# Kernel optimization log

Measured on AMD Instinct MI355X. Metric: run time of the kernel, lower is better.

## Reference

```python
import jax, jax.numpy as jnp
import numpy as np

HIDDEN = 1024
HEADS = 16
HEAD_DIM = HIDDEN // HEADS  # 64
MLP_HIDDEN = int(HIDDEN * 4.0)  # 4096
B, L = 2, 2048
EPS_LN = 1e-6
EPS_RMS = 1e-6


def setup_inputs() -> dict:
    key = jax.random.key(0)
    ks = jax.random.split(key, 12)
    s = 0.02
    return {
        "x": jax.random.normal(ks[0], (B, L, HIDDEN), jnp.float32),
        "vec": jax.random.normal(ks[1], (B, HIDDEN), jnp.float32),
        "pe": jax.random.normal(ks[2], (1, 1, L, HEAD_DIM // 2, 2, 2), jnp.float32),
        "w_mod": jax.random.normal(ks[3], (HIDDEN, 3 * HIDDEN), jnp.float32) * s,
        "b_mod": jnp.zeros((3 * HIDDEN,), jnp.float32),
        "w1": jax.random.normal(ks[4], (HIDDEN, 3 * HIDDEN + MLP_HIDDEN), jnp.float32) * s,
        "b1": jnp.zeros((3 * HIDDEN + MLP_HIDDEN,), jnp.float32),
        "w_mlp": jax.random.normal(ks[5], (MLP_HIDDEN, HIDDEN), jnp.float32) * s,
        "b_mlp": jnp.zeros((HIDDEN,), jnp.float32),
        "w2": jax.random.normal(ks[6], (2 * HIDDEN, HIDDEN), jnp.float32) * s,
        "b2": jnp.zeros((HIDDEN,), jnp.float32),
        "q_scale": jnp.ones((HEAD_DIM,), jnp.float32),
        "k_scale": jnp.ones((HEAD_DIM,), jnp.float32),
    }


def _layernorm(x, eps=EPS_LN):
    m = jnp.mean(x, axis=-1, keepdims=True)
    v = jnp.mean(jnp.square(x - m), axis=-1, keepdims=True)
    return (x - m) * jax.lax.rsqrt(v + eps)


def _rmsnorm(x, scale, eps=EPS_RMS):
    rrms = jax.lax.rsqrt(jnp.mean(jnp.square(x), axis=-1, keepdims=True) + eps)
    return x * rrms * scale


def _apply_rope(t, pe):
    # t: [B,H,L,D]; pe: [1,1,L,D//2,2,2]
    t_ = t.reshape(*t.shape[:-1], -1, 1, 2)  # [B,H,L,D//2,1,2]
    out = pe[..., 0] * t_[..., 0] + pe[..., 1] * t_[..., 1]  # [B,H,L,D//2,2]
    return out.reshape(t.shape)


def reference(x, vec, pe, w_mod, b_mod, w1, b1, w_mlp, b_mlp, w2, b2, q_scale, k_scale):
    # adaLN modulation: silu(vec) -> Dense(3*dim) -> shift, scale, gate
    mod = (jax.nn.silu(vec) @ w_mod + b_mod)[:, None, :]  # [B,1,3H]
    shift, scale, gate = jnp.split(mod, 3, axis=-1)
    x_mod = (1.0 + scale) * _layernorm(x) + shift
    # fused QKV + MLP projection
    h = x_mod @ w1 + b1  # [B,L,3H+MH]
    qkv, mlp = h[..., : 3 * HIDDEN], h[..., 3 * HIDDEN :]
    qkv = qkv.reshape(x.shape[0], x.shape[1], 3, HEADS, HEAD_DIM)
    qkv = jnp.transpose(qkv, (2, 0, 3, 1, 4))  # [3,B,H,L,D]
    q, k, v = qkv[0], qkv[1], qkv[2]
    # QK-RMSNorm per head-dim
    q = _rmsnorm(q, q_scale)
    k = _rmsnorm(k, k_scale)
    # RoPE
    q = _apply_rope(q, pe)
    k = _apply_rope(k, pe)
    # attention
    scores = jnp.einsum("bhqd,bhkd->bhqk", q, k) * (HEAD_DIM ** -0.5)
    probs = jax.nn.softmax(scores, axis=-1)
    attn = jnp.einsum("bhqk,bhkd->bhqd", probs, v)
    attn = jnp.transpose(attn, (0, 2, 1, 3)).reshape(x.shape[0], x.shape[1], HIDDEN)
    # mlp branch (Dense with tanh activation per source) + fused output proj
    mlp_out = jnp.tanh(mlp @ w_mlp + b_mlp)
    out = jnp.concatenate([attn, mlp_out], axis=-1) @ w2 + b2
    return x + gate * out
```

## Files before the change

### kernel.cpp

```cpp
#include <hip/hip_runtime.h>
#include <stdint.h>


#define HID  1024
#define NH   16
#define HD   64
#define MLP  4096
#define D1   7168
#define DQKV 3072
#define DCAT 2048
#define BB   2
#define LL   2048
#define TOK  4096

typedef __attribute__((ext_vector_type(8))) short    bf16x8;
typedef __attribute__((ext_vector_type(4))) float    f32x4;
typedef __attribute__((ext_vector_type(4))) unsigned int u32x4;

__device__ __forceinline__ float b2f(unsigned short u) {
    unsigned int v = ((unsigned int)u) << 16;
    float f; __builtin_memcpy(&f, &v, 4); return f;
}
__device__ __forceinline__ unsigned short f2b(float f) {
    unsigned int v; __builtin_memcpy(&v, &f, 4);
    unsigned int r = (v + 0x7FFFu + ((v >> 16) & 1u)) >> 16;
    return (unsigned short)r;
}
__device__ __forceinline__ unsigned int pkbf2(float a, float b) {
    unsigned int ua, ub;
    __builtin_memcpy(&ua, &a, 4); __builtin_memcpy(&ub, &b, 4);
    return ((ua + 0x8000u) >> 16) | ((ub + 0x8000u) & 0xFFFF0000u);
}
__device__ __forceinline__ void gl_lds16(const unsigned short* g, unsigned short* l) {
    __builtin_amdgcn_global_load_lds(
        (const __attribute__((address_space(1))) unsigned int*)(g),
        (__attribute__((address_space(3))) unsigned int*)(l), 16, 0, 0);
}

__global__ void k_transpose_cvt(const float* __restrict__ in,
                                unsigned short* __restrict__ out, int R, int C) {
    __shared__ float tile[32][33];
    int bx = blockIdx.x, by = blockIdx.y;
    int tx = threadIdx.x, ty = threadIdx.y;
    #pragma unroll
    for (int i = 0; i < 4; i++) {
        int r = by * 32 + ty + i * 8;
        int c = bx * 32 + tx;
        tile[ty + i * 8][tx] = in[(size_t)r * C + c];
    }
    __syncthreads();
    #pragma unroll
    for (int i = 0; i < 4; i++) {
        int ro = bx * 32 + ty + i * 8;
        int co = by * 32 + tx;
        out[(size_t)ro * R + co] = f2b(tile[tx][ty + i * 8]);
    }
}

__global__ void k_vt(const unsigned short* __restrict__ h,
                     unsigned short* __restrict__ vT) {
    __shared__ unsigned short tile[32][33];
    int l0 = blockIdx.x * 32;
    int d0 = (blockIdx.y & 1) * 32;
    int bh = blockIdx.y >> 1;
    int b = bh >> 4, hh = bh & 15;
    int tx = threadIdx.x, ty = threadIdx.y;
    const unsigned short* src = h + ((size_t)(b * LL) + l0) * D1 + 2 * HID + hh * HD + d0;
    #pragma unroll
    for (int i = 0; i < 4; i++)
        tile[ty + i * 8][tx] = src[(size_t)(ty + i * 8) * D1 + tx];
    __syncthreads();
    unsigned short* dst = vT + ((size_t)(b * NH + hh) * HD + d0) * LL + l0;
    #pragma unroll
    for (int i = 0; i < 4; i++)
        dst[(size_t)(ty + i * 8) * LL + tx] = tile[tx][ty + i * 8];
}

__global__ void k_mod(const float* __restrict__ vec,
                      const float* __restrict__ w_mod,
                      const float* __restrict__ b_mod,
                      float* __restrict__ mod) {
    __shared__ float sv[HID];
    __shared__ float red[8][32];
    int b = blockIdx.y, t = threadIdx.x;
    for (int j = t; j < HID; j += 256) {
        float v = vec[b * HID + j];
        sv[j] = v / (1.0f + __expf(-v));
    }
    __syncthreads();
    int n0 = blockIdx.x * 32;
    int on = t & 31, ks = t >> 5;
    float acc = 0.f;
    const float* wp = w_mod + (size_t)(ks * 128) * 3072 + n0 + on;
    #pragma unroll 4
    for (int k = 0; k < 128; k++) acc += sv[ks * 128 + k] * wp[(size_t)k * 3072];
    red[ks][on] = acc;
    __syncthreads();
    if (t < 32) {
        float s = 0.f;
        #pragma unroll
        for (int i = 0; i < 8; i++) s += red[i][t];
        mod[b * 3072 + n0 + t] = s + b_mod[n0 + t];
    }
}

__global__ void k_lnmod(const float* __restrict__ x,
                        const float* __restrict__ mod,
                        unsigned short* __restrict__ xmod) {
    int tok = blockIdx.x;
    int t = threadIdx.x;
    int b = tok >> 11;
    float4 v4 = *(const float4*)(x + (size_t)tok * HID + t * 4);
    float v0 = v4.x, v1 = v4.y, v2 = v4.z, v3 = v4.w;
    float s  = v0 + v1 + v2 + v3;
    float sq = v0*v0 + v1*v1 + v2*v2 + v3*v3;
    for (int off = 1; off < 64; off <<= 1) {
        s  += __shfl_xor(s,  off);
        sq += __shfl_xor(sq, off);
    }
    __shared__ float ls[4], lq[4];
    int w = t >> 6;
    if ((t & 63) == 0) { ls[w] = s; lq[w] = sq; }
    __syncthreads();
    s  = ls[0] + ls[1] + ls[2] + ls[3];
    sq = lq[0] + lq[1] + lq[2] + lq[3];
    float mean = s * (1.0f / HID);
    float var  = sq * (1.0f / HID) - mean * mean;
    float rstd = rsqrtf(var + 1e-6f);
    const float* mb = mod + b * 3072;
    float y[4] = {v0, v1, v2, v3};
    unsigned short r[4];
    #pragma unroll
    for (int j = 0; j < 4; j++) {
        int col = t * 4 + j;
        float nval = (y[j] - mean) * rstd;
        r[j] = f2b((1.0f + mb[1024 + col]) * nval + mb[col]);
    }
    unsigned int o0 = (unsigned int)r[0] | ((unsigned int)r[1] << 16);
    unsigned int o1 = (unsigned int)r[2] | ((unsigned int)r[3] << 16);
    *(uint2*)(xmod + (size_t)tok * HID + t * 4) = make_uint2(o0, o1);
}

template<int EPI>
__global__ __launch_bounds__(256) void k_gemm(
    const unsigned short* __restrict__ A, int lda,
    const unsigned short* __restrict__ Bt, int ldb,
    const float* __restrict__ bias,
    unsigned short* __restrict__ C, float* __restrict__ Cf, int ldc,
    int K,
    const float* __restrict__ xin,
    const float* __restrict__ mod) {
    __shared__ alignas(16) unsigned short As[128 * 64];
    __shared__ alignas(16) unsigned short Bs[128 * 64];
    int t = threadIdx.x;
    int bm = blockIdx.x, bn = blockIdx.y;
    int lane = t & 63, wave = t >> 6;
    int wm = (wave >> 1) * 64, wn = (wave & 1) * 64;
    int ln = lane & 15, quad = lane >> 4;
    int ln7 = ln & 7;

    f32x4 acc[4][4];
    #pragma unroll
    for (int i = 0; i < 4; i++)
        #pragma unroll
        for (int j = 0; j < 4; j++) acc[i][j] = {0.f, 0.f, 0.f, 0.f};

    int sr  = t >> 3;
    int scg = (t & 7) ^ (sr & 7);
    const unsigned short* Ab = A  + (size_t)(bm * 128) * lda;
    const unsigned short* Bb = Bt + (size_t)(bn * 128) * ldb;

    int ksplit = K / gridDim.z;
    int kbeg = blockIdx.z * ksplit, kend = kbeg + ksplit;

    for (int k0 = kbeg; k0 < kend; k0 += 64) {
        __syncthreads();
        #pragma unroll
        for (int c = 0; c < 4; c++) {
            gl_lds16(Ab + (size_t)(c * 32 + sr) * lda + k0 + scg * 8, &As[c * 2048 + t * 8]);
            gl_lds16(Bb + (size_t)(c * 32 + sr) * ldb + k0 + scg * 8, &Bs[c * 2048 + t * 8]);
        }
        __syncthreads();
        #pragma unroll
        for (int ks = 0; ks < 2; ks++) {
            int slot = ((ks * 4 + quad) ^ ln7) * 8;
            bf16x8 af[4], bfr[4];
            #pragma unroll
            for (int i = 0; i < 4; i++)
                af[i] = *(const bf16x8*)(&As[(wm + i * 16 + ln) * 64 + slot]);
            #pragma unroll
            for (int j = 0; j < 4; j++)
                bfr[j] = *(const bf16x8*)(&Bs[(wn + j * 16 + ln) * 64 + slot]);
            #pragma unroll
            for (int i = 0; i < 4; i++)
                #pragma unroll
                for (int j = 0; j < 4; j++)
                    acc[i][j] = __builtin_amdgcn_mfma_f32_16x16x32_bf16(bfr[j], af[i], acc[i][j], 0, 0, 0);
        }
    }

    #pragma unroll
    for (int i = 0; i < 4; i++) {
        #pragma unroll
        for (int j = 0; j < 4; j++) {
            int trow = bm * 128 + wm + i * 16 + ln;
            int ncol = bn * 128 + wn + j * 16 + quad * 4;
            f32x4 a = acc[i][j];
            if (EPI == 3) {
                float4 o = make_float4(a[0], a[1], a[2], a[3]);
                *(float4*)(&Cf[((size_t)blockIdx.z * TOK + trow) * ldc + ncol]) = o;
            } else {
                float4 bv = *(const float4*)(bias + ncol);
                float v0 = a[0] + bv.x, v1 = a[1] + bv.y, v2 = a[2] + bv.z, v3 = a[3] + bv.w;
                if (EPI == 1) { v0 = tanhf(v0); v1 = tanhf(v1); v2 = tanhf(v2); v3 = tanhf(v3); }
                if (EPI == 0 || EPI == 1) {
                    *(uint2*)(&C[(size_t)trow * ldc + ncol]) =
                        make_uint2(pkbf2(v0, v1), pkbf2(v2, v3));
                } else {
                    int b = trow >> 11;
                    float4 gv = *(const float4*)(mod + b * 3072 + 2048 + ncol);
                    float4 xv = *(const float4*)(xin + (size_t)trow * HID + ncol);
                    float4 o = make_float4(xv.x + gv.x * v0, xv.y + gv.y * v1,
                                           xv.z + gv.z * v2, xv.w + gv.w * v3);
                    *(float4*)(&Cf[(size_t)trow * ldc + ncol]) = o;
                }
            }
        }
    }
}

__global__ __launch_bounds__(256) void k_red1(const float* __restrict__ part,
                                              const float* __restrict__ bias,
                                              unsigned short* __restrict__ cat) {
    int idx = blockIdx.x * 256 + threadIdx.x;
    int row = idx >> 8;
    int c4  = (idx & 255) * 4;
    float4 p0 = *(const float4*)(part + (size_t)row * HID + c4);
    float4 p1 = *(const float4*)(part + ((size_t)TOK + row) * HID + c4);
    float4 bv = *(const float4*)(bias + c4);
    float a0 = tanhf(p0.x + p1.x + bv.x);
    float a1 = tanhf(p0.y + p1.y + bv.y);
    float a2 = tanhf(p0.z + p1.z + bv.z);
    float a3 = tanhf(p0.w + p1.w + bv.w);
    *(uint2*)(&cat[(size_t)row * DCAT + HID + c4]) =
        make_uint2(pkbf2(a0, a1), pkbf2(a2, a3));
}

__global__ __launch_bounds__(256) void k_red2(const float* __restrict__ part,
                                              const float* __restrict__ bias,
                                              const float* __restrict__ x,
                                              const float* __restrict__ mod,
                                              float* __restrict__ out) {
    int idx = blockIdx.x * 256 + threadIdx.x;
    int row = idx >> 8;
    int c4  = (idx & 255) * 4;
    int b = row >> 11;
    float4 p0 = *(const float4*)(part + (size_t)row * HID + c4);
    float4 p1 = *(const float4*)(part + ((size_t)TOK + row) * HID + c4);
    float4 bv = *(const float4*)(bias + c4);
    float4 gv = *(const float4*)(mod + b * 3072 + 2048 + c4);
    float4 xv = *(const float4*)(x + (size_t)row * HID + c4);
    float4 o;
    o.x = xv.x + gv.x * (p0.x + p1.x + bv.x);
    o.y = xv.y + gv.y * (p0.y + p1.y + bv.y);
    o.z = xv.z + gv.z * (p0.z + p1.z + bv.z);
    o.w = xv.w + gv.w * (p0.w + p1.w + bv.w);
    *(float4*)(out + (size_t)row * HID + c4) = o;
}

__global__ void k_qkrope(unsigned short* __restrict__ h,
                         const float* __restrict__ pe,
                         const float* __restrict__ q_scale,
                         const float* __restrict__ k_scale) {
    int tok = blockIdx.x;
    int l = tok & (LL - 1);
    int t = threadIdx.x;
    int lane = t & 63, wave = t >> 6;
    int hh = wave * 4 + (lane >> 4);
    int d0 = (lane & 15) * 4;
    unsigned short* row = h + (size_t)tok * D1;
    int i0 = d0 >> 1;
    const float* peb = pe + ((size_t)l * 32 + i0) * 4;
    float4 e0 = *(const float4*)(peb);
    float4 e1 = *(const float4*)(peb + 4);
    #pragma unroll
    for (int qk = 0; qk < 2; qk++) {
        unsigned short* p = row + qk * HID + hh * HD + d0;
        const float* sc = (qk == 0 ? q_scale : k_scale) + d0;
        uint2 qv = *(const uint2*)p;
        float v0 = b2f((unsigned short)(qv.x & 0xFFFF)), v1 = b2f((unsigned short)(qv.x >> 16));
        float v2 = b2f((unsigned short)(qv.y & 0xFFFF)), v3 = b2f((unsigned short)(qv.y >> 16));
        float ssq = v0*v0 + v1*v1 + v2*v2 + v3*v3;
        ssq += __shfl_xor(ssq, 1, 16);
        ssq += __shfl_xor(ssq, 2, 16);
        ssq += __shfl_xor(ssq, 4, 16);
        ssq += __shfl_xor(ssq, 8, 16);
        float rr = rsqrtf(ssq * (1.0f / HD) + 1e-6f);
        if (qk == 0) rr *= 0.18033688011112042f;
        v0 *= rr * sc[0];
        v1 *= rr * sc[1];
        v2 *= rr * sc[2];
        v3 *= rr * sc[3];
        float o0 = e0.x*v0 + e0.y*v1;
        float o1 = e0.z*v0 + e0.w*v1;
        float o2 = e1.x*v2 + e1.y*v3;
        float o3 = e1.z*v2 + e1.w*v3;
        *(uint2*)p = make_uint2(pkbf2(o0, o1), pkbf2(o2, o3));
    }
}

#define KT 64
#define LDP 72
__global__ __launch_bounds__(256) void k_attn(const unsigned short* __restrict__ h,
                                              const unsigned short* __restrict__ vT,
                                              unsigned short* __restrict__ cat) {
    __shared__ alignas(16) unsigned short Ks[KT * 64];
    __shared__ alignas(16) unsigned short Vs[HD * 64];
    __shared__ unsigned short Ps[4 * 16 * LDP];
    int t = threadIdx.x;
    int bx = blockIdx.x;
    int bh = blockIdx.y;
    int b = bh >> 4, hh = bh & 15;
    int lane = t & 63, w = t >> 6;
    int ln = lane & 15, quad = lane >> 4;
    int ln7 = ln & 7;
    const unsigned short* hb = h + (size_t)b * LL * D1;
    const unsigned short* vtb = vT + ((size_t)(b * NH + hh) * HD) * LL;

    bf16x8 qf[2];
    {
        const unsigned short* qbase = hb + (size_t)(bx * 64 + w * 16) * D1 + hh * HD;
        #pragma unroll
        for (int ks = 0; ks < 2; ks++)
            qf[ks] = *(const bf16x8*)(qbase + (size_t)ln * D1 + ks * 32 + quad * 8);
    }

    f32x4 O[4];
    #pragma unroll
    for (int vn = 0; vn < 4; vn++) O[vn] = {0.f, 0.f, 0.f, 0.f};
    float m_ = -1e30f, l_ = 0.f;

    unsigned short* Psw = Ps + w * 16 * LDP;

    int srow = t >> 3;
    int scg  = (t & 7) ^ (srow & 7);

    for (int kb = 0; kb < LL / KT; kb++) {
        __syncthreads();
        {
            const unsigned short* kb0 = hb + (size_t)(kb * KT) * D1 + HID + hh * HD;
            gl_lds16(kb0 + (size_t)srow * D1 + scg * 8,        &Ks[t * 8]);
            gl_lds16(kb0 + (size_t)(srow + 32) * D1 + scg * 8, &Ks[2048 + t * 8]);
            const unsigned short* vb0 = vtb + kb * KT;
            gl_lds16(vb0 + (size_t)srow * LL + scg * 8,        &Vs[t * 8]);
            gl_lds16(vb0 + (size_t)(srow + 32) * LL + scg * 8, &Vs[2048 + t * 8]);
        }
        __syncthreads();

        f32x4 st[4];
        #pragma unroll
        for (int kt = 0; kt < 4; kt++) {
            st[kt] = {0.f, 0.f, 0.f, 0.f};
            #pragma unroll
            for (int ks = 0; ks < 2; ks++) {
                bf16x8 kf = *(const bf16x8*)(&Ks[(kt * 16 + ln) * 64 + (((ks * 4 + quad) ^ ln7) * 8)]);
                st[kt] = __builtin_amdgcn_mfma_f32_16x16x32_bf16(kf, qf[ks], st[kt], 0, 0, 0);
            }
        }

        {
            float p[16];
            float mx = -1e30f;
            #pragma unroll
            for (int kt = 0; kt < 4; kt++)
                #pragma unroll
                for (int r = 0; r < 4; r++) {
                    float v = st[kt][r];
                    p[kt * 4 + r] = v;
                    mx = fmaxf(mx, v);
                }
            mx = fmaxf(mx, __shfl_xor(mx, 16));
            mx = fmaxf(mx, __shfl_xor(mx, 32));
            float mnew = fmaxf(m_, mx);
            float alpha = __builtin_amdgcn_exp2f(m_ - mnew);
            m_ = mnew;
            float sum = 0.f;
            #pragma unroll
            for (int i = 0; i < 16; i++) {
                float e = __builtin_amdgcn_exp2f(p[i] - mnew);
                p[i] = e;
                sum += e;
            }
            sum += __shfl_xor(sum, 16);
            sum += __shfl_xor(sum, 32);
            l_ = l_ * alpha + sum;
            #pragma unroll
            for (int vn = 0; vn < 4; vn++)
                #pragma unroll
                for (int r = 0; r < 4; r++) O[vn][r] *= alpha;
            #pragma unroll
            for (int kt = 0; kt < 4; kt++) {
                unsigned long long pk =
                    (unsigned long long)pkbf2(p[kt*4+0], p[kt*4+1])
                  | ((unsigned long long)pkbf2(p[kt*4+2], p[kt*4+3]) << 32);
                *(unsigned long long*)(&Psw[ln * LDP + kt * 16 + quad * 4]) = pk;
            }
        }

        #pragma unroll
        for (int kt2 = 0; kt2 < 2; kt2++) {
            bf16x8 pb = *(const bf16x8*)(&Psw[ln * LDP + kt2 * 32 + quad * 8]);
            #pragma unroll
            for (int vn = 0; vn < 4; vn++) {
                bf16x8 vf = *(const bf16x8*)(&Vs[(vn * 16 + ln) * 64 + (((kt2 * 4 + quad) ^ ln7) * 8)]);
                O[vn] = __builtin_amdgcn_mfma_f32_16x16x32_bf16(vf, pb, O[vn], 0, 0, 0);
            }
        }
    }

    {
        float rl = 1.0f / l_;
        size_t row = (size_t)(b * LL + bx * 64 + w * 16 + ln);
        #pragma unroll
        for (int vn = 0; vn < 4; vn++) {
            #pragma unroll
            for (int r2 = 0; r2 < 4; r2 += 2) {
                unsigned int pk = pkbf2(O[vn][r2] * rl, O[vn][r2 + 1] * rl);
                *(unsigned int*)(&cat[row * DCAT + hh * HD + vn * 16 + quad * 4 + r2]) = pk;
            }
        }
    }
}

extern "C" void kernel_launch(void* const* d_in, const int* in_sizes, int n_in,
                              void* d_out, int out_size, void* d_ws, size_t ws_size,
                              hipStream_t stream) {
    const float* x       = (const float*)d_in[0];
    const float* vec     = (const float*)d_in[1];
    const float* pe      = (const float*)d_in[2];
    const float* w_mod   = (const float*)d_in[3];
    const float* b_mod   = (const float*)d_in[4];
    const float* w1      = (const float*)d_in[5];
    const float* b1      = (const float*)d_in[6];
    const float* w_mlp   = (const float*)d_in[7];
    const float* b_mlp   = (const float*)d_in[8];
    const float* w2      = (const float*)d_in[9];
    const float* b2      = (const float*)d_in[10];
    const float* q_scale = (const float*)d_in[11];
    const float* k_scale = (const float*)d_in[12];
    float* out = (float*)d_out;

    char* ws = (char*)d_ws;
    size_t off = 0;
    float* mod = (float*)(ws + off);                     off += 6144 * 4;
    unsigned short* xmod  = (unsigned short*)(ws + off); off += (size_t)TOK * HID * 2;
    unsigned short* h     = (unsigned short*)(ws + off); off += (size_t)TOK * D1 * 2;
    unsigned short* cat   = (unsigned short*)(ws + off); off += (size_t)TOK * DCAT * 2;
    unsigned short* w1T   = (unsigned short*)(ws + off); off += (size_t)D1 * HID * 2;
    unsigned short* wmlpT = (unsigned short*)(ws + off); off += (size_t)HID * MLP * 2;
    unsigned short* w2T   = (unsigned short*)(ws + off); off += (size_t)HID * DCAT * 2;
    unsigned short* vTr   = (unsigned short*)(ws + off); off += (size_t)BB * NH * HD * LL * 2;
    float* part = (float*)(ws + off);                    off += (size_t)2 * TOK * HID * 4;

    k_transpose_cvt<<<dim3(D1 / 32, HID / 32), dim3(32, 8), 0, stream>>>(w1, w1T, HID, D1);
    k_transpose_cvt<<<dim3(HID / 32, MLP / 32), dim3(32, 8), 0, stream>>>(w_mlp, wmlpT, MLP, HID);
    k_transpose_cvt<<<dim3(HID / 32, DCAT / 32), dim3(32, 8), 0, stream>>>(w2, w2T, DCAT, HID);

    k_mod<<<dim3(96, BB), 256, 0, stream>>>(vec, w_mod, b_mod, mod);
    k_lnmod<<<TOK, 256, 0, stream>>>(x, mod, xmod);

    k_gemm<0><<<dim3(TOK / 128, D1 / 128), 256, 0, stream>>>(
        xmod, HID, w1T, HID, b1, h, nullptr, D1, HID, nullptr, nullptr);

    k_vt<<<dim3(LL / 32, 2 * BB * NH), dim3(32, 8), 0, stream>>>(h, vTr);
    k_qkrope<<<TOK, 256, 0, stream>>>(h, pe, q_scale, k_scale);

    k_attn<<<dim3(LL / 64, BB * NH), 256, 0, stream>>>(h, vTr, cat);

    k_gemm<3><<<dim3(TOK / 128, HID / 128, 2), 256, 0, stream>>>(
        h + DQKV, D1, wmlpT, MLP, b_mlp, nullptr, part, HID, MLP, nullptr, nullptr);
    k_red1<<<TOK * HID / 1024, 256, 0, stream>>>(part, b_mlp, cat);

    k_gemm<3><<<dim3(TOK / 128, HID / 128, 2), 256, 0, stream>>>(
        cat, DCAT, w2T, DCAT, b2, nullptr, part, HID, DCAT, nullptr, nullptr);
    k_red2<<<TOK * HID / 1024, 256, 0, stream>>>(part, b2, x, mod, out);
}
```

Baseline: 429.0 us.

## Fuse QK RMSNorm, RoPE and V transpose into QKV GEMM epilogue

The first projection GEMM gains a dedicated epilogue that adds bias, then applies per-head RMSNorm and RoPE to the Q and K column blocks in registers. It writes V directly in transposed layout and stores the MLP part normally. This removes the separate V-transpose and qk-rope kernels along with their extra passes over the large h buffer. In exchange, the transposed V stores are strided 2-byte writes, and the epilogue adds register pressure and branching.

```diff
diff --git a/kernel.cpp b/kernel.cpp
--- a/kernel.cpp
+++ b/kernel.cpp
@@ -55,25 +55,6 @@
         int co = by * 32 + tx;
         out[(size_t)ro * R + co] = f2b(tile[tx][ty + i * 8]);
     }
-}
-
-__global__ void k_vt(const unsigned short* __restrict__ h,
-                     unsigned short* __restrict__ vT) {
-    __shared__ unsigned short tile[32][33];
-    int l0 = blockIdx.x * 32;
-    int d0 = (blockIdx.y & 1) * 32;
-    int bh = blockIdx.y >> 1;
-    int b = bh >> 4, hh = bh & 15;
-    int tx = threadIdx.x, ty = threadIdx.y;
-    const unsigned short* src = h + ((size_t)(b * LL) + l0) * D1 + 2 * HID + hh * HD + d0;
-    #pragma unroll
-    for (int i = 0; i < 4; i++)
-        tile[ty + i * 8][tx] = src[(size_t)(ty + i * 8) * D1 + tx];
-    __syncthreads();
-    unsigned short* dst = vT + ((size_t)(b * NH + hh) * HD + d0) * LL + l0;
-    #pragma unroll
-    for (int i = 0; i < 4; i++)
-        dst[(size_t)(ty + i * 8) * LL + tx] = tile[tx][ty + i * 8];
 }
 
 __global__ void k_mod(const float* __restrict__ vec,
@@ -149,7 +130,11 @@
     unsigned short* __restrict__ C, float* __restrict__ Cf, int ldc,
     int K,
     const float* __restrict__ xin,
-    const float* __restrict__ mod) {
+    const float* __restrict__ mod,
+    unsigned short* __restrict__ vT,
+    const float* __restrict__ pe,
+    const float* __restrict__ q_scale,
+    const float* __restrict__ k_scale) {
     __shared__ alignas(16) unsigned short As[128 * 64];
     __shared__ alignas(16) unsigned short Bs[128 * 64];
     int t = threadIdx.x;
@@ -197,6 +182,86 @@
                 for (int j = 0; j < 4; j++)
                     acc[i][j] = __builtin_amdgcn_mfma_f32_16x16x32_bf16(bfr[j], af[i], acc[i][j], 0, 0, 0);
         }
+    }
+
+    if (EPI == 4) {
+        #pragma unroll
+        for (int j = 0; j < 4; j++) {
+            int ncol = bn * 128 + wn + j * 16 + quad * 4;
+            float4 bv = *(const float4*)(bias + ncol);
+            #pragma unroll
+            for (int i = 0; i < 4; i++) {
+                acc[i][j][0] += bv.x; acc[i][j][1] += bv.y;
+                acc[i][j][2] += bv.z; acc[i][j][3] += bv.w;
+            }
+        }
+        int region = bn >> 3;
+        if (region <= 1) {
+            const float* scp = (region == 0) ? q_scale : k_scale;
+            float4 sc4[4];
+            #pragma unroll
+            for (int j = 0; j < 4; j++)
+                sc4[j] = *(const float4*)(scp + j * 16 + quad * 4);
+            #pragma unroll
+            for (int i = 0; i < 4; i++) {
+                int trow = bm * 128 + wm + i * 16 + ln;
+                int l = trow & (LL - 1);
+                float ssq = 0.f;
+                #pragma unroll
+                for (int j = 0; j < 4; j++)
+                    #pragma unroll
+                    for (int r = 0; r < 4; r++) ssq += acc[i][j][r] * acc[i][j][r];
+                ssq += __shfl_xor(ssq, 16);
+                ssq += __shfl_xor(ssq, 32);
+                float rr = rsqrtf(ssq * (1.0f / HD) + 1e-6f);
+                if (region == 0) rr *= 0.18033688011112042f;
+                #pragma unroll
+                for (int j = 0; j < 4; j++) {
+                    float v0 = acc[i][j][0] * rr * sc4[j].x;
+                    float v1 = acc[i][j][1] * rr * sc4[j].y;
+                    float v2 = acc[i][j][2] * rr * sc4[j].z;
+                    float v3 = acc[i][j][3] * rr * sc4[j].w;
+                    const float* peb = pe + ((size_t)l * 32 + j * 8 + quad * 2) * 4;
+                    float4 e0 = *(const float4*)(peb);
+                    float4 e1 = *(const float4*)(peb + 4);
+                    float o0 = e0.x * v0 + e0.y * v1;
+                    float o1 = e0.z * v0 + e0.w * v1;
+                    float o2 = e1.x * v2 + e1.y * v3;
+                    float o3 = e1.z * v2 + e1.w * v3;
+                    int ncol = bn * 128 + wn + j * 16 + quad * 4;
+                    *(uint2*)(&C[(size_t)trow * ldc + ncol]) =
+                        make_uint2(pkbf2(o0, o1), pkbf2(o2, o3));
+                }
+            }
+        } else if (region == 2) {
+            int hh = (bn * 128 + wn - 2048) >> 6;
+            #pragma unroll
+            for (int i = 0; i < 4; i++) {
+                int trow = bm * 128 + wm + i * 16 + ln;
+                int b = trow >> 11, l = trow & (LL - 1);
+                unsigned short* dstb = vT + ((size_t)(b * NH + hh) * HD) * LL + l;
+                #pragma unroll
+                for (int j = 0; j < 4; j++) {
+                    int d0 = j * 16 + quad * 4;
+                    #pragma unroll
+                    for (int r = 0; r < 4; r++)
+                        dstb[(size_t)(d0 + r) * LL] = f2b(acc[i][j][r]);
+                }
+            }
+        } else {
+            #pragma unroll
+            for (int i = 0; i < 4; i++) {
+                int trow = bm * 128 + wm + i * 16 + ln;
+                #pragma unroll
+                for (int j = 0; j < 4; j++) {
+                    int ncol = bn * 128 + wn + j * 16 + quad * 4;
+                    *(uint2*)(&C[(size_t)trow * ldc + ncol]) =
+                        make_uint2(pkbf2(acc[i][j][0], acc[i][j][1]),
+                                   pkbf2(acc[i][j][2], acc[i][j][3]));
+                }
+            }
+        }
+        return;
     }
 
     #pragma unroll
@@ -213,7 +278,7 @@
                 float4 bv = *(const float4*)(bias + ncol);
                 float v0 = a[0] + bv.x, v1 = a[1] + bv.y, v2 = a[2] + bv.z, v3 = a[3] + bv.w;
                 if (EPI == 1) { v0 = tanhf(v0); v1 = tanhf(v1); v2 = tanhf(v2); v3 = tanhf(v3); }
-                if (EPI == 0 || EPI == 1) {
+                if (EPI == 1) {
                     *(uint2*)(&C[(size_t)trow * ldc + ncol]) =
                         make_uint2(pkbf2(v0, v1), pkbf2(v2, v3));
                 } else {
@@ -268,47 +333,6 @@
     *(float4*)(out + (size_t)row * HID + c4) = o;
 }
 
-__global__ void k_qkrope(unsigned short* __restrict__ h,
-                         const float* __restrict__ pe,
-                         const float* __restrict__ q_scale,
-                         const float* __restrict__ k_scale) {
-    int tok = blockIdx.x;
-    int l = tok & (LL - 1);
-    int t = threadIdx.x;
-    int lane = t & 63, wave = t >> 6;
-    int hh = wave * 4 + (lane >> 4);
-    int d0 = (lane & 15) * 4;
-    unsigned short* row = h + (size_t)tok * D1;
-    int i0 = d0 >> 1;
-    const float* peb = pe + ((size_t)l * 32 + i0) * 4;
-    float4 e0 = *(const float4*)(peb);
-    float4 e1 = *(const float4*)(peb + 4);
-    #pragma unroll
-    for (int qk = 0; qk < 2; qk++) {
-        unsigned short* p = row + qk * HID + hh * HD + d0;
-        const float* sc = (qk == 0 ? q_scale : k_scale) + d0;
-        uint2 qv = *(const uint2*)p;
-        float v0 = b2f((unsigned short)(qv.x & 0xFFFF)), v1 = b2f((unsigned short)(qv.x >> 16));
-        float v2 = b2f((unsigned short)(qv.y & 0xFFFF)), v3 = b2f((unsigned short)(qv.y >> 16));
-        float ssq = v0*v0 + v1*v1 + v2*v2 + v3*v3;
-        ssq += __shfl_xor(ssq, 1, 16);
-        ssq += __shfl_xor(ssq, 2, 16);
-        ssq += __shfl_xor(ssq, 4, 16);
-        ssq += __shfl_xor(ssq, 8, 16);
-        float rr = rsqrtf(ssq * (1.0f / HD) + 1e-6f);
-        if (qk == 0) rr *= 0.18033688011112042f;
-        v0 *= rr * sc[0];
-        v1 *= rr * sc[1];
-        v2 *= rr * sc[2];
-        v3 *= rr * sc[3];
-        float o0 = e0.x*v0 + e0.y*v1;
-        float o1 = e0.z*v0 + e0.w*v1;
-        float o2 = e1.x*v2 + e1.y*v3;
-        float o3 = e1.z*v2 + e1.w*v3;
-        *(uint2*)p = make_uint2(pkbf2(o0, o1), pkbf2(o2, o3));
-    }
-}
-
 #define KT 64
 #define LDP 72
 __global__ __launch_bounds__(256) void k_attn(const unsigned short* __restrict__ h,
@@ -469,19 +493,19 @@
     k_mod<<<dim3(96, BB), 256, 0, stream>>>(vec, w_mod, b_mod, mod);
     k_lnmod<<<TOK, 256, 0, stream>>>(x, mod, xmod);
 
-    k_gemm<0><<<dim3(TOK / 128, D1 / 128), 256, 0, stream>>>(
-        xmod, HID, w1T, HID, b1, h, nullptr, D1, HID, nullptr, nullptr);
-
-    k_vt<<<dim3(LL / 32, 2 * BB * NH), dim3(32, 8), 0, stream>>>(h, vTr);
-    k_qkrope<<<TOK, 256, 0, stream>>>(h, pe, q_scale, k_scale);
+    k_gemm<4><<<dim3(TOK / 128, D1 / 128), 256, 0, stream>>>(
+        xmod, HID, w1T, HID, b1, h, nullptr, D1, HID, nullptr, nullptr,
+        vTr, pe, q_scale, k_scale);
 
     k_attn<<<dim3(LL / 64, BB * NH), 256, 0, stream>>>(h, vTr, cat);
 
     k_gemm<3><<<dim3(TOK / 128, HID / 128, 2), 256, 0, stream>>>(
-        h + DQKV, D1, wmlpT, MLP, b_mlp, nullptr, part, HID, MLP, nullptr, nullptr);
+        h + DQKV, D1, wmlpT, MLP, b_mlp, nullptr, part, HID, MLP, nullptr, nullptr,
+        nullptr, nullptr, nullptr, nullptr);
     k_red1<<<TOK * HID / 1024, 256, 0, stream>>>(part, b_mlp, cat);
 
     k_gemm<3><<<dim3(TOK / 128, HID / 128, 2), 256, 0, stream>>>(
-        cat, DCAT, w2T, DCAT, b2, nullptr, part, HID, DCAT, nullptr, nullptr);
+        cat, DCAT, w2T, DCAT, b2, nullptr, part, HID, DCAT, nullptr, nullptr,
+        nullptr, nullptr, nullptr, nullptr);
     k_red2<<<TOK * HID / 1024, 256, 0, stream>>>(part, b2, x, mod, out);
 }
```

Result: no change. 426.9 us (-0.5%).
